# Performance work log

Measured on AMD Instinct MI355X. Metric: run time of the kernel, lower is better.

## Reference

```python
import jax, jax.numpy as jnp
import numpy as np

N_NODES = 50000


def _sage_conv(x, src, dst, Wl, Wr, b):
    # PyG SAGEConv (aggr='mean'): out = lin_l(mean_{j in N(i)} x_j) + lin_r(x_i)
    msgs = x[src]                                              # [E, d] gather
    s = jax.ops.segment_sum(msgs, dst, num_segments=N_NODES)   # [N, d]
    cnt = jax.ops.segment_sum(jnp.ones((src.shape[0], 1), x.dtype), dst,
                              num_segments=N_NODES)            # [N, 1]
    agg = s / jnp.maximum(cnt, 1.0)                            # mean, 0 if no nbrs
    return agg @ Wl.T + x @ Wr.T + b


def setup_inputs() -> dict:
    key = jax.random.key(0)
    ks = jax.random.split(key, 12)
    in_dim, h = 128, 128
    E, P = 500000, 200000
    x = jax.random.normal(ks[0], (N_NODES, in_dim), dtype=jnp.float32)
    edge_index = jax.random.randint(ks[1], (2, E), 0, N_NODES)
    pairs = jax.random.randint(ks[2], (P, 2), 0, N_NODES)
    def lin(k, fan_out, fan_in):
        bound = 1.0 / np.sqrt(fan_in)
        return jax.random.uniform(k, (fan_out, fan_in), jnp.float32, -bound, bound)
    return {
        "x": x, "edge_index": edge_index, "pairs": pairs,
        "Wl1": lin(ks[3], h, in_dim), "Wr1": lin(ks[4], h, in_dim),
        "b1": jnp.zeros((h,), jnp.float32),
        "Wl2": lin(ks[5], h, h), "Wr2": lin(ks[6], h, h),
        "b2": jnp.zeros((h,), jnp.float32),
        "W3": lin(ks[7], h, 2 * h), "b3": jnp.zeros((h,), jnp.float32),
        "W4": lin(ks[8], 1, h), "b4": jnp.zeros((1,), jnp.float32),
    }


def reference(x, edge_index, pairs, Wl1, Wr1, b1, Wl2, Wr2, b2, W3, b3, W4, b4):
    src, dst = edge_index[0], edge_index[1]
    h1 = jax.nn.relu(_sage_conv(x, src, dst, Wl1, Wr1, b1))    # [N, h]
    h2 = jax.nn.relu(_sage_conv(h1, src, dst, Wl2, Wr2, b2))   # [N, h]
    a = h2[pairs[:, 0]]                                        # [P, h]
    b = h2[pairs[:, 1]]                                        # [P, h]
    z = jnp.concatenate([a, b], axis=1)                        # [P, 2h]
    s = jax.nn.relu(z @ W3.T + b3) @ W4.T + b4                 # [P, 1]
    return jax.nn.sigmoid(s).squeeze(-1)                       # [P]
```

## Files before the change

kernel.cpp:

```cpp
#include <hip/hip_runtime.h>
#include <math.h>

#define N_NODES 50000
#define E_EDGES 500000
#define P_PAIRS 200000
#define MAX_DEG 64

#define NB        196
#define EB        2048
#define EPT       8
#define SORT_BLKS 245

typedef __bf16    bf16x8 __attribute__((ext_vector_type(8)));
typedef __bf16    bf16x4 __attribute__((ext_vector_type(4)));
typedef _Float16  f16x8  __attribute__((ext_vector_type(8)));
typedef float     f32x4  __attribute__((ext_vector_type(4)));


#define CONV_BLKS 1563
#define PREP_BLKS 128

__global__ __launch_bounds__(256) void pre_k(
        const float* __restrict__ x, __bf16* __restrict__ xb,
        const int* __restrict__ dst,
        int* __restrict__ bucketCnt, int* __restrict__ blockBase,
        const float* __restrict__ Wl1, const float* __restrict__ Wr1,
        const float* __restrict__ Wl2, const float* __restrict__ Wr2,
        const float* __restrict__ W3,
        __bf16* __restrict__ P1, __bf16* __restrict__ P2, __bf16* __restrict__ P4) {
    __shared__ int cnt[NB];
    int b = blockIdx.x, t = threadIdx.x;
    if (b < SORT_BLKS) {
        if (t < NB) cnt[t] = 0;
        __syncthreads();
        int ebase = b * EB;
        #pragma unroll
        for (int i = 0; i < EPT; ++i) {
            int e = ebase + i * 256 + t;
            if (e < E_EDGES) atomicAdd(&cnt[dst[e] >> 8], 1);
        }
        __syncthreads();
        if (t < NB) blockBase[b * NB + t] = atomicAdd(&bucketCnt[t], cnt[t]);
    } else if (b < SORT_BLKS + CONV_BLKS) {
        int i0 = (b - SORT_BLKS) * 1024 + t;
        #pragma unroll
        for (int k = 0; k < 4; ++k) {
            int i = i0 + k * 256;
            if (i < N_NODES * 128 / 4) {
                float4 v = ((const float4*)x)[i];
                bf16x4 o;
                o[0] = (__bf16)v.x; o[1] = (__bf16)v.y;
                o[2] = (__bf16)v.z; o[3] = (__bf16)v.w;
                *(bf16x4*)(xb + (size_t)i * 4) = o;
            }
        }
    } else {
        int i = (b - SORT_BLKS - CONV_BLKS) * 256 + t;
        int lane = (i >> 3) & 63;
        int j = i & 7;
        int kq = (lane >> 4) * 8 + j;
        {
            int kt = i >> 12, nt = (i >> 9) & 7;
            int n = nt * 16 + (lane & 15);
            int k = kt * 32 + kq;
            P1[i] = (__bf16)((k < 128) ? Wl1[n * 128 + k] : Wr1[n * 128 + (k - 128)]);
            P2[i] = (__bf16)((k < 128) ? Wl2[n * 128 + k] : Wr2[n * 128 + (k - 128)]);
        }
        {
            int kt = i >> 13, nt = (i >> 9) & 15;
            int n = nt * 16 + (lane & 15);
            int k = kt * 32 + kq;
            P4[i] = (__bf16)((n < 128) ? W3[n * 256 + k] : W3[(n - 128) * 256 + 128 + k]);
        }
    }
}


__global__ __launch_bounds__(256) void place_k(const int* __restrict__ src,
                                               const int* __restrict__ dst,
                                               const int* __restrict__ bucketCnt,
                                               const int* __restrict__ blockBase,
                                               unsigned* __restrict__ edgebuf) {
    __shared__ int cnt[256];
    __shared__ int buf[256];
    __shared__ int sbase[NB];
    __shared__ int gbase[NB];
    __shared__ int cur[NB];
    __shared__ unsigned sortbuf[EB];
    __shared__ unsigned char bktof[EB];
    int blk = blockIdx.x, t = threadIdx.x;

    int bv = (t < NB) ? bucketCnt[t] : 0;
    buf[t] = bv;
    __syncthreads();
    for (int off = 1; off < 256; off <<= 1) {
        int xv = (t >= off) ? buf[t - off] : 0;
        __syncthreads();
        buf[t] += xv;
        __syncthreads();
    }
    if (t < NB) gbase[t] = (buf[t] - bv) + blockBase[blk * NB + t];
    cnt[t] = 0;
    if (t < NB) cur[t] = 0;
    __syncthreads();

    unsigned packed[EPT];
    int bk[EPT];
    int ebase = blk * EB;
    #pragma unroll
    for (int i = 0; i < EPT; ++i) {
        int e = ebase + i * 256 + t;
        if (e < E_EDGES) {
            int d = dst[e];
            packed[i] = ((unsigned)d << 16) | (unsigned)src[e];
            bk[i] = d >> 8;
            atomicAdd(&cnt[bk[i]], 1);
        } else bk[i] = -1;
    }
    __syncthreads();

    int v = cnt[t];
    buf[t] = v;
    __syncthreads();
    for (int off = 1; off < 256; off <<= 1) {
        int xv = (t >= off) ? buf[t - off] : 0;
        __syncthreads();
        buf[t] += xv;
        __syncthreads();
    }
    if (t < NB) sbase[t] = buf[t] - v;
    __syncthreads();

    #pragma unroll
    for (int i = 0; i < EPT; ++i) {
        if (bk[i] >= 0) {
            int p = sbase[bk[i]] + atomicAdd(&cur[bk[i]], 1);
            sortbuf[p] = packed[i];
            bktof[p] = (unsigned char)bk[i];
        }
    }
    __syncthreads();

    int nE = E_EDGES - ebase; if (nE > EB) nE = EB;
    for (int i = t; i < nE; i += 256) {
        int bb = bktof[i];
        edgebuf[gbase[bb] + (i - sbase[bb])] = sortbuf[i];
    }
}


__global__ __launch_bounds__(256) void slots_k(const unsigned* __restrict__ edgebuf,
                                               const int* __restrict__ bucketCnt,
                                               unsigned short* __restrict__ slots,
                                               int* __restrict__ deg) {
    __shared__ unsigned short srow[256 * MAX_DEG];
    __shared__ int cur[256];
    __shared__ int buf[256];
    __shared__ int sc[2];
    int b = blockIdx.x, t = threadIdx.x;

    int bv = (t < NB) ? bucketCnt[t] : 0;
    buf[t] = bv;
    cur[t] = 0;
    __syncthreads();
    for (int off = 1; off < 256; off <<= 1) {
        int xv = (t >= off) ? buf[t - off] : 0;
        __syncthreads();
        buf[t] += xv;
        __syncthreads();
    }
    if (t == b) { sc[0] = buf[t] - bv; sc[1] = bv; }
    __syncthreads();
    int base = sc[0], n = sc[1];

    for (int i = t; i < n; i += 256) {
        unsigned p = edgebuf[base + i];
        int dl = (p >> 16) & 255;
        int pos = atomicAdd(&cur[dl], 1);
        if (pos < MAX_DEG) srow[dl * MAX_DEG + pos] = (unsigned short)(p & 0xFFFFu);
    }
    __syncthreads();
    const int4* sr16 = (const int4*)srow;
    int4* sl16 = (int4*)slots;
    int gbase16 = b * 2048;
    for (int i = t; i < 2048; i += 256) {
        int node = b * 256 + (i >> 3);
        if (node < N_NODES) sl16[gbase16 + i] = sr16[i];
    }
    int node = b * 256 + t;
    if (node < N_NODES) deg[node] = cur[t];
}


__global__ __launch_bounds__(256) void agg1_k(const __bf16* __restrict__ feat,
                                              const int* __restrict__ deg_a,
                                              const unsigned short* __restrict__ slots,
                                              __bf16* __restrict__ agg) {
    int n = blockIdx.x * 4 + (threadIdx.x >> 6);
    if (n >= N_NODES) return;
    int lane = threadIdx.x & 63;
    int slot = lane >> 4, l = lane & 15;
    int deg = deg_a[n];
    int nit = (deg < MAX_DEG) ? deg : MAX_DEG;

    int ed = (int)slots[n * MAX_DEG + lane];

    float s[8];
    #pragma unroll
    for (int e = 0; e < 8; ++e) s[e] = 0.f;

    int batches = (nit + 15) >> 4;
    int eb = slot;
    for (int b = 0; b < batches; ++b, eb += 16) {
        int sn0 = __builtin_amdgcn_ds_bpermute(eb << 2, ed);
        int sn1 = __builtin_amdgcn_ds_bpermute((eb + 4) << 2, ed);
        int sn2 = __builtin_amdgcn_ds_bpermute((eb + 8) << 2, ed);
        int sn3 = __builtin_amdgcn_ds_bpermute((eb + 12) << 2, ed);
        bf16x8 v0 = *(const bf16x8*)(feat + (size_t)sn0 * 128 + l * 8);
        bf16x8 v1 = *(const bf16x8*)(feat + (size_t)sn1 * 128 + l * 8);
        bf16x8 v2 = *(const bf16x8*)(feat + (size_t)sn2 * 128 + l * 8);
        bf16x8 v3 = *(const bf16x8*)(feat + (size_t)sn3 * 128 + l * 8);
        if (eb < nit) {
            #pragma unroll
            for (int e = 0; e < 8; ++e) s[e] += (float)v0[e];
        }
        if (eb + 4 < nit) {
            #pragma unroll
            for (int e = 0; e < 8; ++e) s[e] += (float)v1[e];
        }
        if (eb + 8 < nit) {
            #pragma unroll
            for (int e = 0; e < 8; ++e) s[e] += (float)v2[e];
        }
        if (eb + 12 < nit) {
            #pragma unroll
            for (int e = 0; e < 8; ++e) s[e] += (float)v3[e];
        }
    }

    #pragma unroll
    for (int e = 0; e < 8; ++e) {
        s[e] += __shfl_xor(s[e], 16, 64);
        s[e] += __shfl_xor(s[e], 32, 64);
    }

    if (slot == 0) {
        float inv = 1.0f / fmaxf((float)deg, 1.0f);
        bf16x8 o;
        #pragma unroll
        for (int e = 0; e < 8; ++e) o[e] = (__bf16)(s[e] * inv);
        *(bf16x8*)(agg + (size_t)n * 128 + l * 8) = o;
    }
}


__global__ __launch_bounds__(256) void layer_mfma_k(const __bf16* __restrict__ agg,
                                                    const __bf16* __restrict__ feat,
                                                    const __bf16* __restrict__ wpack,
                                                    const float* __restrict__ bias,
                                                    __bf16* __restrict__ out) {
    int wave = threadIdx.x >> 6;
    int lane = threadIdx.x & 63;
    int m = lane & 15, quad = lane >> 4;
    int rbase = blockIdx.x * 64 + wave * 16;
    int r0 = rbase + m; if (r0 > N_NODES - 1) r0 = N_NODES - 1;

    f32x4 acc[8];
    #pragma unroll
    for (int nt = 0; nt < 8; ++nt) acc[nt] = (f32x4)0.f;

    #pragma unroll
    for (int kt = 0; kt < 8; ++kt) {
        const __bf16* src = (kt < 4) ? agg : feat;
        int ko = (kt & 3) * 32 + quad * 8;
        bf16x8 a0 = *(const bf16x8*)(src + (size_t)r0 * 128 + ko);
        const __bf16* wb = wpack + (size_t)kt * 4096 + lane * 8;
        #pragma unroll
        for (int nt = 0; nt < 8; ++nt) {
            bf16x8 b = *(const bf16x8*)(wb + nt * 512);
            acc[nt] = __builtin_amdgcn_mfma_f32_16x16x32_bf16(a0, b, acc[nt], 0, 0, 0);
        }
    }

    #pragma unroll
    for (int r = 0; r < 4; ++r) {
        int row = rbase + quad * 4 + r;
        if (row < N_NODES) {
            #pragma unroll
            for (int nt = 0; nt < 8; ++nt) {
                float v = acc[nt][r] + bias[nt * 16 + m];
                out[(size_t)row * 128 + nt * 16 + m] = (__bf16)fmaxf(v, 0.f);
            }
        }
    }
}


__global__ __launch_bounds__(256) void layer2uv_k(const __bf16* __restrict__ agg,
                                                  const __bf16* __restrict__ feat,
                                                  const __bf16* __restrict__ wpack,
                                                  const float* __restrict__ bias,
                                                  const __bf16* __restrict__ wpack4,
                                                  _Float16* __restrict__ UV) {
    __shared__ __bf16 sh[4][16][136];
    int wave = threadIdx.x >> 6;
    int lane = threadIdx.x & 63;
    int m = lane & 15, q = lane >> 4;
    int rbase = blockIdx.x * 64 + wave * 16;
    int r0 = rbase + m; if (r0 > N_NODES - 1) r0 = N_NODES - 1;

    f32x4 acc[8];
    #pragma unroll
    for (int nt = 0; nt < 8; ++nt) acc[nt] = (f32x4)0.f;

    #pragma unroll
    for (int kt = 0; kt < 8; ++kt) {
        const __bf16* src = (kt < 4) ? agg : feat;
        int ko = (kt & 3) * 32 + q * 8;
        bf16x8 a0 = *(const bf16x8*)(src + (size_t)r0 * 128 + ko);
        const __bf16* wb = wpack + (size_t)kt * 4096 + lane * 8;
        #pragma unroll
        for (int nt = 0; nt < 8; ++nt) {
            bf16x8 b = *(const bf16x8*)(wb + nt * 512);
            acc[nt] = __builtin_amdgcn_mfma_f32_16x16x32_bf16(a0, b, acc[nt], 0, 0, 0);
        }
    }

    #pragma unroll
    for (int rr = 0; rr < 4; ++rr)
        #pragma unroll
        for (int nt = 0; nt < 8; ++nt) {
            float v = acc[nt][rr] + bias[nt * 16 + m];
            sh[wave][q * 4 + rr][nt * 16 + m] = (__bf16)fmaxf(v, 0.f);
        }

    f32x4 acc2[16];
    #pragma unroll
    for (int nt = 0; nt < 16; ++nt) acc2[nt] = (f32x4)0.f;

    #pragma unroll
    for (int kt = 0; kt < 4; ++kt) {
        bf16x8 a = *(const bf16x8*)&sh[wave][m][kt * 32 + q * 8];
        const __bf16* wb = wpack4 + (size_t)kt * 8192 + lane * 8;
        #pragma unroll
        for (int nt = 0; nt < 16; ++nt) {
            bf16x8 b = *(const bf16x8*)(wb + nt * 512);
            acc2[nt] = __builtin_amdgcn_mfma_f32_16x16x32_bf16(a, b, acc2[nt], 0, 0, 0);
        }
    }

    #pragma unroll
    for (int rr = 0; rr < 4; ++rr) {
        int row = rbase + q * 4 + rr;
        if (row < N_NODES) {
            #pragma unroll
            for (int nt = 0; nt < 16; ++nt)
                UV[(size_t)row * 256 + nt * 16 + m] = (_Float16)acc2[nt][rr];
        }
    }
}


__global__ __launch_bounds__(256) void pair_ep_k(const _Float16* __restrict__ UV,
                                                 const int* __restrict__ pairs,
                                                 const float* __restrict__ b3,
                                                 const float* __restrict__ W4,
                                                 const float* __restrict__ b4,
                                                 float* __restrict__ out) {
    int t = threadIdx.x;
    int g = t >> 4, l = t & 15;
    int base = blockIdx.x * 64;

    float4 b3a = *(const float4*)(b3 + l * 8);
    float4 b3b = *(const float4*)(b3 + l * 8 + 4);
    float4 w4a = *(const float4*)(W4 + l * 8);
    float4 w4b = *(const float4*)(W4 + l * 8 + 4);
    float bb[8] = {b3a.x, b3a.y, b3a.z, b3a.w, b3b.x, b3b.y, b3b.z, b3b.w};
    float ww[8] = {w4a.x, w4a.y, w4a.z, w4a.w, w4b.x, w4b.y, w4b.z, w4b.w};
    float b4s = b4[0];

    int2 pr[4];
    #pragma unroll
    for (int i = 0; i < 4; ++i) pr[i] = ((const int2*)pairs)[base + i * 16 + g];

    f16x8 ua[4], vb[4];
    #pragma unroll
    for (int i = 0; i < 4; ++i) {
        ua[i] = *(const f16x8*)(UV + (size_t)pr[i].x * 256 + l * 8);
        vb[i] = *(const f16x8*)(UV + (size_t)pr[i].y * 256 + 128 + l * 8);
    }

    #pragma unroll
    for (int i = 0; i < 4; ++i) {
        float p = 0.f;
        #pragma unroll
        for (int e = 0; e < 8; ++e)
            p += fmaxf((float)ua[i][e] + (float)vb[i][e] + bb[e], 0.f) * ww[e];
        #pragma unroll
        for (int s = 1; s < 16; s <<= 1) p += __shfl_xor(p, s, 64);
        if (l == 0)
            out[base + i * 16 + g] = 1.0f / (1.0f + expf(-(p + b4s)));
    }
}


extern "C" void kernel_launch(void* const* d_in, const int* in_sizes, int n_in,
                              void* d_out, int out_size, void* d_ws, size_t ws_size,
                              hipStream_t stream) {
    const float* x   = (const float*)d_in[0];
    const int*   ei  = (const int*)d_in[1];
    const int*   prs = (const int*)d_in[2];
    const float* Wl1 = (const float*)d_in[3];
    const float* Wr1 = (const float*)d_in[4];
    const float* b1  = (const float*)d_in[5];
    const float* Wl2 = (const float*)d_in[6];
    const float* Wr2 = (const float*)d_in[7];
    const float* b2  = (const float*)d_in[8];
    const float* W3  = (const float*)d_in[9];
    const float* b3  = (const float*)d_in[10];
    const float* W4  = (const float*)d_in[11];
    const float* b4  = (const float*)d_in[12];
    float* out = (float*)d_out;

    const int* srcv = ei;
    const int* dstv = ei + E_EDGES;

    char* ws = (char*)d_ws;
    size_t off = 0;
    auto alloc = [&](size_t bytes) -> void* {
        void* p = ws + off;
        off = (off + bytes + 255) & ~(size_t)255;
        return p;
    };
    int*            bucketCnt  = (int*)alloc(sizeof(int) * NB);
    int*            blockBase  = (int*)alloc(sizeof(int) * SORT_BLKS * NB);
    unsigned*       edgebuf    = (unsigned*)alloc(sizeof(unsigned) * E_EDGES);
    int*            deg        = (int*)alloc(sizeof(int) * N_NODES);
    unsigned short* slots      = (unsigned short*)alloc(sizeof(unsigned short) * (size_t)N_NODES * MAX_DEG + 512);
    __bf16*   P1     = (__bf16*)alloc(sizeof(__bf16) * 32768);
    __bf16*   P2     = (__bf16*)alloc(sizeof(__bf16) * 32768);
    __bf16*   P4     = (__bf16*)alloc(sizeof(__bf16) * 32768);
    __bf16*   xb     = (__bf16*)alloc(sizeof(__bf16) * (size_t)N_NODES * 128);
    __bf16*   aggb   = (__bf16*)alloc(sizeof(__bf16) * (size_t)N_NODES * 128);
    __bf16*   h1b    = (__bf16*)alloc(sizeof(__bf16) * (size_t)N_NODES * 128);
    _Float16* UV     = (_Float16*)alloc(sizeof(_Float16) * (size_t)N_NODES * 256);
    (void)ws_size; (void)in_sizes; (void)n_in; (void)out_size;

    hipMemsetAsync(bucketCnt, 0, sizeof(int) * NB, stream);

    pre_k<<<SORT_BLKS + CONV_BLKS + PREP_BLKS, 256, 0, stream>>>(
        x, xb, dstv, bucketCnt, blockBase, Wl1, Wr1, Wl2, Wr2, W3, P1, P2, P4);
    place_k<<<SORT_BLKS, 256, 0, stream>>>(srcv, dstv, bucketCnt, blockBase, edgebuf);
    slots_k<<<NB, 256, 0, stream>>>(edgebuf, bucketCnt, slots, deg);

    agg1_k<<<(N_NODES + 3) / 4, 256, 0, stream>>>(xb, deg, slots, aggb);
    layer_mfma_k<<<(N_NODES + 63) / 64, 256, 0, stream>>>(aggb, xb, P1, b1, h1b);
    agg1_k<<<(N_NODES + 3) / 4, 256, 0, stream>>>(h1b, deg, slots, aggb);
    layer2uv_k<<<(N_NODES + 63) / 64, 256, 0, stream>>>(aggb, h1b, P2, b2, P4, UV);
    pair_ep_k<<<P_PAIRS / 64, 256, 0, stream>>>(UV, prs, b3, W4, b4, out);
}
```

Before: 217.3 us.

## Replace bucket sort edge CSR build with direct global atomic scatter

```diff
diff --git a/kernel.cpp b/kernel.cpp
--- a/kernel.cpp
+++ b/kernel.cpp
@@ -6,43 +6,36 @@
 #define P_PAIRS 200000
 #define MAX_DEG 64
 
-#define NB        196
-#define EB        2048
-#define EPT       8
-#define SORT_BLKS 245
-
 typedef __bf16    bf16x8 __attribute__((ext_vector_type(8)));
 typedef __bf16    bf16x4 __attribute__((ext_vector_type(4)));
 typedef _Float16  f16x8  __attribute__((ext_vector_type(8)));
 typedef float     f32x4  __attribute__((ext_vector_type(4)));
 
 
+#define SCAT_BLKS 1954
 #define CONV_BLKS 1563
 #define PREP_BLKS 128
 
 __global__ __launch_bounds__(256) void pre_k(
         const float* __restrict__ x, __bf16* __restrict__ xb,
-        const int* __restrict__ dst,
-        int* __restrict__ bucketCnt, int* __restrict__ blockBase,
+        const int* __restrict__ src, const int* __restrict__ dst,
+        int* __restrict__ deg, unsigned short* __restrict__ slots,
         const float* __restrict__ Wl1, const float* __restrict__ Wr1,
         const float* __restrict__ Wl2, const float* __restrict__ Wr2,
         const float* __restrict__ W3,
         __bf16* __restrict__ P1, __bf16* __restrict__ P2, __bf16* __restrict__ P4) {
-    __shared__ int cnt[NB];
     int b = blockIdx.x, t = threadIdx.x;
-    if (b < SORT_BLKS) {
-        if (t < NB) cnt[t] = 0;
-        __syncthreads();
-        int ebase = b * EB;
-        #pragma unroll
-        for (int i = 0; i < EPT; ++i) {
-            int e = ebase + i * 256 + t;
-            if (e < E_EDGES) atomicAdd(&cnt[dst[e] >> 8], 1);
-        }
-        __syncthreads();
-        if (t < NB) blockBase[b * NB + t] = atomicAdd(&bucketCnt[t], cnt[t]);
-    } else if (b < SORT_BLKS + CONV_BLKS) {
-        int i0 = (b - SORT_BLKS) * 1024 + t;
+    if (b < SCAT_BLKS) {
+        int e = b * 256 + t;
+        if (e < E_EDGES) {
+            int d = dst[e];
+            int s = src[e];
+            int pos = atomicAdd(&deg[d], 1);
+            if (pos < MAX_DEG)
+                slots[(size_t)d * MAX_DEG + pos] = (unsigned short)s;
+        }
+    } else if (b < SCAT_BLKS + CONV_BLKS) {
+        int i0 = (b - SCAT_BLKS) * 1024 + t;
         #pragma unroll
         for (int k = 0; k < 4; ++k) {
             int i = i0 + k * 256;
@@ -55,7 +48,7 @@
             }
         }
     } else {
-        int i = (b - SORT_BLKS - CONV_BLKS) * 256 + t;
+        int i = (b - SCAT_BLKS - CONV_BLKS) * 256 + t;
         int lane = (i >> 3) & 63;
         int j = i & 7;
         int kq = (lane >> 4) * 8 + j;
@@ -73,122 +66,6 @@
             P4[i] = (__bf16)((n < 128) ? W3[n * 256 + k] : W3[(n - 128) * 256 + 128 + k]);
         }
     }
-}
-
-
-__global__ __launch_bounds__(256) void place_k(const int* __restrict__ src,
-                                               const int* __restrict__ dst,
-                                               const int* __restrict__ bucketCnt,
-                                               const int* __restrict__ blockBase,
-                                               unsigned* __restrict__ edgebuf) {
-    __shared__ int cnt[256];
-    __shared__ int buf[256];
-    __shared__ int sbase[NB];
-    __shared__ int gbase[NB];
-    __shared__ int cur[NB];
-    __shared__ unsigned sortbuf[EB];
-    __shared__ unsigned char bktof[EB];
-    int blk = blockIdx.x, t = threadIdx.x;
-
-    int bv = (t < NB) ? bucketCnt[t] : 0;
-    buf[t] = bv;
-    __syncthreads();
-    for (int off = 1; off < 256; off <<= 1) {
-        int xv = (t >= off) ? buf[t - off] : 0;
-        __syncthreads();
-        buf[t] += xv;
-        __syncthreads();
-    }
-    if (t < NB) gbase[t] = (buf[t] - bv) + blockBase[blk * NB + t];
-    cnt[t] = 0;
-    if (t < NB) cur[t] = 0;
-    __syncthreads();
-
-    unsigned packed[EPT];
-    int bk[EPT];
-    int ebase = blk * EB;
-    #pragma unroll
-    for (int i = 0; i < EPT; ++i) {
-        int e = ebase + i * 256 + t;
-        if (e < E_EDGES) {
-            int d = dst[e];
-            packed[i] = ((unsigned)d << 16) | (unsigned)src[e];
-            bk[i] = d >> 8;
-            atomicAdd(&cnt[bk[i]], 1);
-        } else bk[i] = -1;
-    }
-    __syncthreads();
-
-    int v = cnt[t];
-    buf[t] = v;
-    __syncthreads();
-    for (int off = 1; off < 256; off <<= 1) {
-        int xv = (t >= off) ? buf[t - off] : 0;
-        __syncthreads();
-        buf[t] += xv;
-        __syncthreads();
-    }
-    if (t < NB) sbase[t] = buf[t] - v;
-    __syncthreads();
-
-    #pragma unroll
-    for (int i = 0; i < EPT; ++i) {
-        if (bk[i] >= 0) {
-            int p = sbase[bk[i]] + atomicAdd(&cur[bk[i]], 1);
-            sortbuf[p] = packed[i];
-            bktof[p] = (unsigned char)bk[i];
-        }
-    }
-    __syncthreads();
-
-    int nE = E_EDGES - ebase; if (nE > EB) nE = EB;
-    for (int i = t; i < nE; i += 256) {
-        int bb = bktof[i];
-        edgebuf[gbase[bb] + (i - sbase[bb])] = sortbuf[i];
-    }
-}
-
-
-__global__ __launch_bounds__(256) void slots_k(const unsigned* __restrict__ edgebuf,
-                                               const int* __restrict__ bucketCnt,
-                                               unsigned short* __restrict__ slots,
-                                               int* __restrict__ deg) {
-    __shared__ unsigned short srow[256 * MAX_DEG];
-    __shared__ int cur[256];
-    __shared__ int buf[256];
-    __shared__ int sc[2];
-    int b = blockIdx.x, t = threadIdx.x;
-
-    int bv = (t < NB) ? bucketCnt[t] : 0;
-    buf[t] = bv;
-    cur[t] = 0;
-    __syncthreads();
-    for (int off = 1; off < 256; off <<= 1) {
-        int xv = (t >= off) ? buf[t - off] : 0;
-        __syncthreads();
-        buf[t] += xv;
-        __syncthreads();
-    }
-    if (t == b) { sc[0] = buf[t] - bv; sc[1] = bv; }
-    __syncthreads();
-    int base = sc[0], n = sc[1];
-
-    for (int i = t; i < n; i += 256) {
-        unsigned p = edgebuf[base + i];
-        int dl = (p >> 16) & 255;
-        int pos = atomicAdd(&cur[dl], 1);
-        if (pos < MAX_DEG) srow[dl * MAX_DEG + pos] = (unsigned short)(p & 0xFFFFu);
-    }
-    __syncthreads();
-    const int4* sr16 = (const int4*)srow;
-    int4* sl16 = (int4*)slots;
-    int gbase16 = b * 2048;
-    for (int i = t; i < 2048; i += 256) {
-        int node = b * 256 + (i >> 3);
-        if (node < N_NODES) sl16[gbase16 + i] = sr16[i];
-    }
-    int node = b * 256 + t;
-    if (node < N_NODES) deg[node] = cur[t];
 }
 
 
@@ -432,11 +309,8 @@
         off = (off + bytes + 255) & ~(size_t)255;
         return p;
     };
-    int*            bucketCnt  = (int*)alloc(sizeof(int) * NB);
-    int*            blockBase  = (int*)alloc(sizeof(int) * SORT_BLKS * NB);
-    unsigned*       edgebuf    = (unsigned*)alloc(sizeof(unsigned) * E_EDGES);
-    int*            deg        = (int*)alloc(sizeof(int) * N_NODES);
-    unsigned short* slots      = (unsigned short*)alloc(sizeof(unsigned short) * (size_t)N_NODES * MAX_DEG + 512);
+    int*            deg    = (int*)alloc(sizeof(int) * N_NODES);
+    unsigned short* slots  = (unsigned short*)alloc(sizeof(unsigned short) * (size_t)N_NODES * MAX_DEG + 512);
     __bf16*   P1     = (__bf16*)alloc(sizeof(__bf16) * 32768);
     __bf16*   P2     = (__bf16*)alloc(sizeof(__bf16) * 32768);
     __bf16*   P4     = (__bf16*)alloc(sizeof(__bf16) * 32768);
@@ -446,12 +320,10 @@
     _Float16* UV     = (_Float16*)alloc(sizeof(_Float16) * (size_t)N_NODES * 256);
     (void)ws_size; (void)in_sizes; (void)n_in; (void)out_size;
 
-    hipMemsetAsync(bucketCnt, 0, sizeof(int) * NB, stream);
-
-    pre_k<<<SORT_BLKS + CONV_BLKS + PREP_BLKS, 256, 0, stream>>>(
-        x, xb, dstv, bucketCnt, blockBase, Wl1, Wr1, Wl2, Wr2, W3, P1, P2, P4);
-    place_k<<<SORT_BLKS, 256, 0, stream>>>(srcv, dstv, bucketCnt, blockBase, edgebuf);
-    slots_k<<<NB, 256, 0, stream>>>(edgebuf, bucketCnt, slots, deg);
+    hipMemsetAsync(deg, 0, sizeof(int) * N_NODES, stream);
+
+    pre_k<<<SCAT_BLKS + CONV_BLKS + PREP_BLKS, 256, 0, stream>>>(
+        x, xb, srcv, dstv, deg, slots, Wl1, Wr1, Wl2, Wr2, W3, P1, P2, P4);
 
     agg1_k<<<(N_NODES + 3) / 4, 256, 0, stream>>>(xb, deg, slots, aggb);
     layer_mfma_k<<<(N_NODES + 63) / 64, 256, 0, stream>>>(aggb, xb, P1, b1, h1b);
```

After: 222.0 us. 1.02x slower.
